# Optimization experiments

Measured on AMD Instinct MI355X. Metric: run time of the kernel, lower is better.

## Reference

```python
import jax, jax.numpy as jnp
import numpy as np

H, D = 4, 32            # heads, per-head dim (hidden = H*D = 128)
HID = H * D
OUT = 64
NC, ND, E = 50000, 50000, 400000
FC, FD = 256, 256


def setup_inputs() -> dict:
    key = jax.random.key(0)
    ks = iter(jax.random.split(key, 64))

    def n(shape, s=0.05):
        return jax.random.normal(next(ks), shape, dtype=jnp.float32) * s

    def ei(n_src, n_dst):
        return jnp.stack([jax.random.randint(next(ks), (E,), 0, n_src),
                          jax.random.randint(next(ks), (E,), 0, n_dst)]).astype(jnp.int32)

    inp = {
        'x_concept': n((NC, FC), 1.0),
        'x_doc': n((ND, FD), 1.0),
        'ei_cc': ei(NC, NC),
        'ei_dc': ei(ND, NC),
        'ei_cd': ei(NC, ND),
        # conv1 params
        'W1c': n((FC, HID)), 'b1c': n((HID,)),
        'W1d': n((FD, HID)), 'b1d': n((HID,)),
        'a1s_cc': n((H, D)), 'a1d_cc': n((H, D)),
        'a1s_dc': n((H, D)), 'a1d_dc': n((H, D)),
        'a1s_cd': n((H, D)), 'a1d_cd': n((H, D)),
        'k1W': n((HID, HID)), 'k1b': n((HID,)), 'q1': n((HID,)),
        # conv2 params
        'W2c': n((HID, HID)), 'b2c': n((HID,)),
        'W2d': n((HID, HID)), 'b2d': n((HID,)),
        'a2s_cc': n((H, D)), 'a2d_cc': n((H, D)),
        'a2s_dc': n((H, D)), 'a2d_dc': n((H, D)),
        'a2s_cd': n((H, D)), 'a2d_cd': n((H, D)),
        'k2W': n((HID, HID)), 'k2b': n((HID,)), 'q2': n((HID,)),
        # final projection
        'pW': n((HID, OUT)), 'pb': n((OUT,)),
    }
    return inp


def _seg_softmax(logit, idx, n):
    # PyG softmax: exp(x - max_per_segment) / (sum_per_segment + 1e-16)
    m = jax.ops.segment_max(logit, idx, num_segments=n)
    e = jnp.exp(logit - m[idx])
    s = jax.ops.segment_sum(e, idx, num_segments=n)
    return e / (s[idx] + 1e-16)


def _edge_att(h_src, h_dst, a_s, a_d, src, dst, n_dst):
    # h_src: [Ns,H,D]; GAT-style per-edge attention, softmax over dst
    logit = jax.nn.leaky_relu((h_src * a_s).sum(-1)[src] + (h_dst * a_d).sum(-1)[dst], 0.2)
    alpha = _seg_softmax(logit, dst, n_dst)                     # [E,H]
    out = jax.ops.segment_sum(h_src[src] * alpha[:, :, None], dst, num_segments=n_dst)
    return jax.nn.relu(out.reshape(n_dst, H * D))


def _group(outs, kW, kb, q):
    # semantic attention across relation types
    stk = jnp.stack(outs)                                       # [T,N,C]
    score = (q * jnp.tanh(stk @ kW + kb).mean(axis=1)).sum(-1)  # [T]
    w = jax.nn.softmax(score)
    return jnp.einsum('t,tnc->nc', w, stk)


def _han_layer(xc, xd, Wc, bc, Wd, bd, as_cc, ad_cc, as_dc, ad_dc, as_cd, ad_cd,
               kW, kb, q, ei_cc, ei_dc, ei_cd):
    hc = (xc @ Wc + bc).reshape(-1, H, D)
    hd = (xd @ Wd + bd).reshape(-1, H, D)
    nc, nd = hc.shape[0], hd.shape[0]
    o_cc = _edge_att(hc, hc, as_cc, ad_cc, ei_cc[0], ei_cc[1], nc)
    o_dc = _edge_att(hd, hc, as_dc, ad_dc, ei_dc[0], ei_dc[1], nc)
    o_cd = _edge_att(hc, hd, as_cd, ad_cd, ei_cd[0], ei_cd[1], nd)
    return _group([o_cc, o_dc], kW, kb, q), _group([o_cd], kW, kb, q)


def reference(x_concept, x_doc, ei_cc, ei_dc, ei_cd,
              W1c, b1c, W1d, b1d, a1s_cc, a1d_cc, a1s_dc, a1d_dc, a1s_cd, a1d_cd, k1W, k1b, q1,
              W2c, b2c, W2d, b2d, a2s_cc, a2d_cc, a2s_dc, a2d_dc, a2s_cd, a2d_cd, k2W, k2b, q2,
              pW, pb):
    c, d = _han_layer(x_concept, x_doc, W1c, b1c, W1d, b1d,
                      a1s_cc, a1d_cc, a1s_dc, a1d_dc, a1s_cd, a1d_cd,
                      k1W, k1b, q1, ei_cc, ei_dc, ei_cd)
    c, d = jax.nn.elu(c), jax.nn.elu(d)
    c, d = _han_layer(c, d, W2c, b2c, W2d, b2d,
                      a2s_cc, a2d_cc, a2s_dc, a2d_dc, a2s_cd, a2d_cd,
                      k2W, k2b, q2, ei_cc, ei_dc, ei_cd)
    c, d = jax.nn.elu(c), jax.nn.elu(d)
    pc = c @ pW + pb
    pd = d @ pW + pb
    # F.normalize(p=2) on 'concept' only
    pc = pc / jnp.maximum(jnp.linalg.norm(pc, axis=-1, keepdims=True), 1e-12)
    return pc, pd
```

## Files before the change

### kernel.cpp

```cpp
#include <hip/hip_runtime.h>
#include <hip/hip_fp16.h>
#include <cmath>

#define DEVI static __device__ __forceinline__

constexpr int HIDn = 128, OUTn = 64;
constexpr int NCn = 50000, NDn = 50000, En = 400000;
constexpr int SCAN_N = 150000, SCAN_BLK = 1024;
constexpr int SCAN_NB = (SCAN_N + SCAN_BLK - 1) / SCAN_BLK;

typedef __attribute__((ext_vector_type(8))) short bf16x8;
typedef __attribute__((ext_vector_type(4))) float f32x4;

DEVI unsigned fmap(float f) {
  int i = __float_as_int(f);
  return (i < 0) ? ~((unsigned)i) : (((unsigned)i) | 0x80000000u);
}
DEVI float fdecode(unsigned u) {
  int i = (u & 0x80000000u) ? (int)(u & 0x7fffffffu) : (int)(~u);
  return __int_as_float(i);
}

DEVI float tanh_fast(float x) {
  float e = __expf(2.f * x);
  return 1.f - __fdividef(2.f, e + 1.f);
}

DEVI unsigned short f2bf(float x) {
  unsigned u = __float_as_uint(x);
  return (unsigned short)((u + 0x7FFFu + ((u >> 16) & 1u)) >> 16);
}
DEVI float bf2f(unsigned short h) {
  unsigned u = ((unsigned)h) << 16;
  return __uint_as_float(u);
}

template<int MODE, int HALF>
DEVI void loadrow8(float* __restrict__ tmp,
                   const void* __restrict__ A, const void* __restrict__ A2,
                   float w2, float w3, size_t base)
{
  float v[8];
  if (HALF) {
    float4 raw = *(const float4*)((const __half*)A + base);
    const __half2* h2 = (const __half2*)&raw;
    #pragma unroll
    for (int j = 0; j < 4; ++j) {
      float2 f = __half22float2(h2[j]);
      v[2 * j] = f.x; v[2 * j + 1] = f.y;
    }
  } else {
    const float4* p = (const float4*)((const float*)A + base);
    float4 u0 = p[0], u1 = p[1];
    v[0] = u0.x; v[1] = u0.y; v[2] = u0.z; v[3] = u0.w;
    v[4] = u1.x; v[5] = u1.y; v[6] = u1.z; v[7] = u1.w;
  }
  if (MODE == 2) {
    float vb[8];
    if (HALF) {
      float4 raw = *(const float4*)((const __half*)A2 + base);
      const __half2* h2 = (const __half2*)&raw;
      #pragma unroll
      for (int j = 0; j < 4; ++j) {
        float2 f = __half22float2(h2[j]);
        vb[2 * j] = f.x; vb[2 * j + 1] = f.y;
      }
    } else {
      const float4* q = (const float4*)((const float*)A2 + base);
      float4 t0 = q[0], t1 = q[1];
      vb[0] = t0.x; vb[1] = t0.y; vb[2] = t0.z; vb[3] = t0.w;
      vb[4] = t1.x; vb[5] = t1.y; vb[6] = t1.z; vb[7] = t1.w;
    }
    #pragma unroll
    for (int i = 0; i < 8; ++i) v[i] = w2 * v[i] + w3 * vb[i];
  }
  if (MODE >= 1) {
    #pragma unroll
    for (int i = 0; i < 8; ++i) v[i] = (v[i] > 0.f) ? v[i] : (__expf(v[i]) - 1.f);
  }
  #pragma unroll
  for (int i = 0; i < 8; ++i) tmp[i] = v[i];
}

template<int MODE, int HALF>
DEVI bf16x8 packrow8(const void* __restrict__ A, const void* __restrict__ A2,
                     float w2, float w3, size_t base)
{
  float t[8];
  loadrow8<MODE, HALF>(t, A, A2, w2, w3, base);
  bf16x8 r;
  #pragma unroll
  for (int i = 0; i < 8; ++i) r[i] = (short)f2bf(t[i]);
  return r;
}

template<int KI, int MODEc, int MODEd, int IN16, int OUT16>
__global__ __launch_bounds__(256)
void gemm2_mfma(const void* __restrict__ Ac, const void* __restrict__ Ac2,
                const float* __restrict__ wv,
                const unsigned short* __restrict__ WcH, const unsigned short* __restrict__ WcL,
                const float* __restrict__ bc, void* __restrict__ Cc,
                const void* __restrict__ Ad,
                const unsigned short* __restrict__ WdH, const unsigned short* __restrict__ WdL,
                const float* __restrict__ bd, void* __restrict__ Cd,
                int N,
                const float* __restrict__ avc0, const float* __restrict__ avc1,
                const float* __restrict__ avc2, const float* __restrict__ avc3,
                const float* __restrict__ avd0, const float* __restrict__ avd1,
                float* __restrict__ doc0, float* __restrict__ doc1,
                float* __restrict__ doc2, float* __restrict__ doc3,
                float* __restrict__ dod0, float* __restrict__ dod1)
{
  __shared__ float As[64][36];
  __shared__ unsigned short Bh[128][40];
  __shared__ unsigned short Bl[128][40];
  constexpr int NC = KI / 32;
  const bool isC = (blockIdx.y == 0);
  const void* A  = isC ? Ac : Ad;
  const void* A2 = isC ? Ac2 : nullptr;
  const unsigned short* Wh = isC ? WcH : WdH;
  const unsigned short* Wl = isC ? WcL : WdL;
  const float* bias = isC ? bc : bd;
  void* Cv = isC ? Cc : Cd;
  float w2 = 0.f, w3 = 0.f;
  if (MODEc == 2) { if (isC) { w2 = wv[2]; w3 = wv[3]; } }

  const int tid = threadIdx.x;
  const int w = tid >> 6, lane = tid & 63;
  const int m = lane & 15, b4 = lane >> 4;
  const int row0 = blockIdx.x * 64;
  const int row0w = row0 + w * 16;

  const int rA = tid >> 2, kqA = (tid & 3) << 3;
  const int rowA = row0 + rA;
  const int cB = tid >> 1, kqB = (tid & 1) << 4;

  f32x4 acc[8];
  #pragma unroll
  for (int t = 0; t < 8; ++t) acc[t] = (f32x4){0.f, 0.f, 0.f, 0.f};

  float tA[8];
  float4 bh0, bh1, bl0, bl1;

  auto loadA = [&](int k0) {
    if (rowA < N) {
      if (isC) loadrow8<MODEc, IN16>(tA, A, A2, w2, w3, (size_t)rowA * KI + k0 + kqA);
      else     loadrow8<MODEd, IN16>(tA, A, nullptr, 0.f, 0.f, (size_t)rowA * KI + k0 + kqA);
    } else {
      #pragma unroll
      for (int i = 0; i < 8; ++i) tA[i] = 0.f;
    }
  };
  auto loadB = [&](int k0) {
    const float4* ph = (const float4*)(Wh + (size_t)cB * KI + k0 + kqB);
    const float4* pl = (const float4*)(Wl + (size_t)cB * KI + k0 + kqB);
    bh0 = ph[0]; bh1 = ph[1]; bl0 = pl[0]; bl1 = pl[1];
  };

  loadA(0);
  loadB(0);

  for (int c = 0; c < NC; ++c) {
    *(float4*)&As[rA][kqA]     = make_float4(tA[0], tA[1], tA[2], tA[3]);
    *(float4*)&As[rA][kqA + 4] = make_float4(tA[4], tA[5], tA[6], tA[7]);
    *(float4*)&Bh[cB][kqB]     = bh0;
    *(float4*)&Bh[cB][kqB + 8] = bh1;
    *(float4*)&Bl[cB][kqB]     = bl0;
    *(float4*)&Bl[cB][kqB + 8] = bl1;
    __syncthreads();

    if (c + 1 < NC) {
      loadA((c + 1) * 32);
      loadB((c + 1) * 32);
    }

    bf16x8 ah, al;
    {
      const float* ap = &As[w * 16 + m][b4 * 8];
      float4 u0 = *(const float4*)ap;
      float4 u1 = *(const float4*)(ap + 4);
      float t8[8] = {u0.x, u0.y, u0.z, u0.w, u1.x, u1.y, u1.z, u1.w};
      #pragma unroll
      for (int i = 0; i < 8; ++i) {
        unsigned short h = f2bf(t8[i]);
        ah[i] = (short)h;
        al[i] = (short)f2bf(t8[i] - bf2f(h));
      }
    }
    #pragma unroll
    for (int t = 0; t < 8; ++t) {
      const int col = t * 16 + m;
      bf16x8 bh = *(const bf16x8*)&Bh[col][b4 * 8];
      bf16x8 bl = *(const bf16x8*)&Bl[col][b4 * 8];
      acc[t] = __builtin_amdgcn_mfma_f32_16x16x32_bf16(ah, bh, acc[t], 0, 0, 0);
      acc[t] = __builtin_amdgcn_mfma_f32_16x16x32_bf16(al, bh, acc[t], 0, 0, 0);
      acc[t] = __builtin_amdgcn_mfma_f32_16x16x32_bf16(ah, bl, acc[t], 0, 0, 0);
    }
    __syncthreads();
  }

  float bt[8];
  #pragma unroll
  for (int t = 0; t < 8; ++t) bt[t] = bias[t * 16 + m];

  #pragma unroll
  for (int t = 0; t < 8; ++t) {
    const int col = t * 16 + m;
    #pragma unroll
    for (int r = 0; r < 4; ++r) {
      const int row = row0w + b4 * 4 + r;
      if (row < N) {
        float v = acc[t][r] + bt[t];
        if (OUT16) ((__half*)Cv)[(size_t)row * 128 + col] = __float2half(v);
        else       ((float*)Cv)[(size_t)row * 128 + col] = v;
      }
    }
  }

  const float* avp[4];
  float* dop[4];
  int nv;
  if (isC) {
    avp[0] = avc0; avp[1] = avc1; avp[2] = avc2; avp[3] = avc3;
    dop[0] = doc0; dop[1] = doc1; dop[2] = doc2; dop[3] = doc3; nv = 4;
  } else {
    avp[0] = avd0; avp[1] = avd1; avp[2] = avd0; avp[3] = avd1;
    dop[0] = dod0; dop[1] = dod1; dop[2] = dod0; dop[3] = dod1; nv = 2;
  }
  float avv[4][8];
  #pragma unroll
  for (int v = 0; v < 4; ++v) {
    if (v < nv) {
      #pragma unroll
      for (int t = 0; t < 8; ++t) avv[v][t] = avp[v][t * 16 + m];
    }
  }
  #pragma unroll
  for (int h = 0; h < 4; ++h) {
    #pragma unroll
    for (int v = 0; v < 4; ++v) {
      if (v < nv) {
        #pragma unroll
        for (int r = 0; r < 4; ++r) {
          float p = (acc[2 * h][r] + bt[2 * h]) * avv[v][2 * h]
                  + (acc[2 * h + 1][r] + bt[2 * h + 1]) * avv[v][2 * h + 1];
          p += __shfl_xor(p, 1);
          p += __shfl_xor(p, 2);
          p += __shfl_xor(p, 4);
          p += __shfl_xor(p, 8);
          if (m == 0) {
            const int row = row0w + b4 * 4 + r;
            if (row < N) dop[v][(size_t)row * 4 + h] = p;
          }
        }
      }
    }
  }
}

__global__ void hist3(const int* __restrict__ ei0, const int* __restrict__ ei1,
                      const int* __restrict__ ei2, int* __restrict__ deg)
{
  int gid = blockIdx.x * blockDim.x + threadIdx.x;
  if (gid >= 3 * En) return;
  int g = gid / En, e = gid - g * En;
  const int* ei = (g == 0) ? ei0 : (g == 1) ? ei1 : ei2;
  atomicAdd(&deg[g * 50000 + ei[En + e]], 1);
}

__global__ void scan_pass1(const int* __restrict__ deg, int* __restrict__ incl,
                           int* __restrict__ bsum)
{
  __shared__ int wsum[16];
  int tid = threadIdx.x;
  int gid = blockIdx.x * SCAN_BLK + tid;
  int v = (gid < SCAN_N) ? deg[gid] : 0;
  int lane = tid & 63, w = tid >> 6;
  int x = v;
  #pragma unroll
  for (int off = 1; off < 64; off <<= 1) {
    int y = __shfl_up(x, off);
    if (lane >= off) x += y;
  }
  if (lane == 63) wsum[w] = x;
  __syncthreads();
  if (tid == 0) {
    int s = 0;
    #pragma unroll
    for (int ww = 0; ww < 16; ++ww) { int t = wsum[ww]; wsum[ww] = s; s += t; }
    bsum[blockIdx.x] = s;
  }
  __syncthreads();
  x += wsum[w];
  if (gid < SCAN_N) incl[gid] = x;
}

__global__ void scan_pass2(int* __restrict__ bsum, int nb)
{
  __shared__ int wsum[16];
  int tid = threadIdx.x;
  int v = (tid < nb) ? bsum[tid] : 0;
  int lane = tid & 63, w = tid >> 6;
  int x = v;
  #pragma unroll
  for (int off = 1; off < 64; off <<= 1) {
    int y = __shfl_up(x, off);
    if (lane >= off) x += y;
  }
  if (lane == 63) wsum[w] = x;
  __syncthreads();
  if (tid == 0) {
    int s = 0;
    #pragma unroll
    for (int ww = 0; ww < 16; ++ww) { int t = wsum[ww]; wsum[ww] = s; s += t; }
  }
  __syncthreads();
  x += wsum[w];
  if (tid < nb) bsum[tid] = x - v;
}

__global__ void scan_pass3(const int* __restrict__ incl, const int* __restrict__ bsum,
                           int* __restrict__ offs)
{
  int gid = blockIdx.x * SCAN_BLK + threadIdx.x;
  if (gid == 0) offs[0] = 0;
  if (gid < SCAN_N) offs[gid + 1] = incl[gid] + bsum[gid / SCAN_BLK];
}

__global__ void fill3(const int* __restrict__ ei0, const int* __restrict__ ei1,
                      const int* __restrict__ ei2, const int* __restrict__ offs,
                      int* __restrict__ cursor, int* __restrict__ elist)
{
  int gid = blockIdx.x * blockDim.x + threadIdx.x;
  if (gid >= 3 * En) return;
  int g = gid / En, e = gid - g * En;
  const int* ei = (g == 0) ? ei0 : (g == 1) ? ei1 : ei2;
  int s = ei[e], d = g * 50000 + ei[En + e];
  int p = atomicAdd(&cursor[d], 1);
  elist[offs[d] + p] = s;
}

__global__ void wprep(const float* __restrict__ k1W, const float* __restrict__ k2W,
                      const float* __restrict__ pW,
                      const float* __restrict__ W1c, const float* __restrict__ W1d,
                      const float* __restrict__ W2c, const float* __restrict__ W2d,
                      unsigned short* kW1t, unsigned short* kW2t, unsigned short* pWt,
                      unsigned short* W1cH, unsigned short* W1cL,
                      unsigned short* W1dH, unsigned short* W1dL,
                      unsigned short* W2cH, unsigned short* W2cL,
                      unsigned short* W2dH, unsigned short* W2dL)
{
  int gid = blockIdx.x * 256 + threadIdx.x;
  if (gid < 16384) {
    int k = gid >> 7, c = gid & 127;
    kW1t[(size_t)c * 128 + k] = f2bf(k1W[gid]);
  } else if (gid < 32768) {
    int i = gid - 16384, k = i >> 7, c = i & 127;
    kW2t[(size_t)c * 128 + k] = f2bf(k2W[i]);
  } else if (gid < 40960) {
    int i = gid - 32768, k = i / 64, c = i - k * 64;
    pWt[(size_t)c * 128 + k] = f2bf(pW[i]);
  } else if (gid < 73728) {
    int i = gid - 40960, k = i >> 7, c = i & 127;
    float v = W1c[i]; unsigned short h = f2bf(v);
    W1cH[(size_t)c * 256 + k] = h;
    W1cL[(size_t)c * 256 + k] = f2bf(v - bf2f(h));
  } else if (gid < 106496) {
    int i = gid - 73728, k = i >> 7, c = i & 127;
    float v = W1d[i]; unsigned short h = f2bf(v);
    W1dH[(size_t)c * 256 + k] = h;
    W1dL[(size_t)c * 256 + k] = f2bf(v - bf2f(h));
  } else if (gid < 122880) {
    int i = gid - 106496, k = i >> 7, c = i & 127;
    float v = W2c[i]; unsigned short h = f2bf(v);
    W2cH[(size_t)c * 128 + k] = h;
    W2cL[(size_t)c * 128 + k] = f2bf(v - bf2f(h));
  } else if (gid < 139264) {
    int i = gid - 122880, k = i >> 7, c = i & 127;
    float v = W2d[i]; unsigned short h = f2bf(v);
    W2dH[(size_t)c * 128 + k] = h;
    W2dL[(size_t)c * 128 + k] = f2bf(v - bf2f(h));
  }
}

struct EdgeOp {
  const int* offs; const int* elist;
  const float* sdot; const float* ddot;
  const __half* hsrc; __half* out;
};

DEVI void csr_att_body(const EdgeOp& op, int dst, int lane)
{
  const int i0 = op.offs[dst], i1 = op.offs[dst + 1];
  const int hB = lane >> 4;
  const float ddv = op.ddot[dst * 4 + hB];
  const __half* hsrc = op.hsrc;
  const float* sdot = op.sdot;
  const int* el = op.elist;
  const int wsel = lane & 48;
  float den = 0.f, a0 = 0.f, a1 = 0.f;

  for (int base = i0; base < i1; base += 16) {
    int i = base + (lane & 15);
    int s_ = 0;
    float w = 0.f;
    if (i < i1) {
      s_ = el[i];
      float lv = sdot[s_ * 4 + hB] + ddv;
      lv = fminf(fmaxf(lv, 0.2f * lv), 80.f);
      w = __expf(lv);
    }
    float g = w;
    g += __shfl_xor(g, 1);
    g += __shfl_xor(g, 2);
    g += __shfl_xor(g, 4);
    g += __shfl_xor(g, 8);
    den += g;

    const int rem = min(16, i1 - base);
    int j = 0;
    for (; j + 2 <= rem; j += 2) {
      int sA = __shfl(s_, j);
      int sB = __shfl(s_, j + 1);
      float wA = __shfl(w, wsel | j);
      float wB = __shfl(w, wsel | (j + 1));
      float2 hA = __half22float2(*(const __half2*)(hsrc + (size_t)sA * HIDn + lane * 2));
      float2 hBv = __half22float2(*(const __half2*)(hsrc + (size_t)sB * HIDn + lane * 2));
      a0 += hA.x * wA + hBv.x * wB;
      a1 += hA.y * wA + hBv.y * wB;
    }
    if (j < rem) {
      int sA = __shfl(s_, j);
      float wA = __shfl(w, wsel | j);
      float2 hA = __half22float2(*(const __half2*)(hsrc + (size_t)sA * HIDn + lane * 2));
      a0 += hA.x * wA;
      a1 += hA.y * wA;
    }
  }
  float dinv = __fdividef(1.f, den + 1e-16f);
  __half2 o2 = __floats2half2_rn(fmaxf(a0 * dinv, 0.f), fmaxf(a1 * dinv, 0.f));
  *(__half2*)(op.out + (size_t)dst * HIDn + lane * 2) = o2;
}

__global__ __launch_bounds__(256)
void csr_att3(EdgeOp op0, EdgeOp op1, EdgeOp op2, int Ndst)
{
  int wave = (blockIdx.x * 256 + threadIdx.x) >> 6;
  if (wave >= Ndst) return;
  const int lane = threadIdx.x & 63;
  if (blockIdx.y == 0)      csr_att_body(op0, wave, lane);
  else if (blockIdx.y == 1) csr_att_body(op1, wave, lane);
  else                      csr_att_body(op2, wave, lane);
}

__global__ void edge_logit_max(const int* __restrict__ ei,
                               const float* __restrict__ sdot,
                               const float* __restrict__ ddot,
                               unsigned* __restrict__ m)
{
  int e = blockIdx.x * blockDim.x + threadIdx.x;
  if (e >= En) return;
  int s = ei[e], d = ei[En + e];
  #pragma unroll
  for (int hh = 0; hh < 4; ++hh) {
    float l = sdot[s * 4 + hh] + ddot[d * 4 + hh];
    l = (l > 0.f) ? l : 0.2f * l;
    atomicMax(&m[d * 4 + hh], fmap(l));
  }
}

__global__ void edge_exp_sum(const int* __restrict__ ei,
                             const float* __restrict__ sdot,
                             const float* __restrict__ ddot,
                             const unsigned* __restrict__ m,
                             float* __restrict__ sden,
                             float* __restrict__ ebuf)
{
  int e = blockIdx.x * blockDim.x + threadIdx.x;
  if (e >= En) return;
  int s = ei[e], d = ei[En + e];
  #pragma unroll
  for (int hh = 0; hh < 4; ++hh) {
    float l = sdot[s * 4 + hh] + ddot[d * 4 + hh];
    l = (l > 0.f) ? l : 0.2f * l;
    float ex = expf(fminf(l - fdecode(m[d * 4 + hh]), 0.f));
    ebuf[e * 4 + hh] = ex;
    atomicAdd(&sden[d * 4 + hh], ex);
  }
}

__global__ __launch_bounds__(256)
void edge_scatter(const int* __restrict__ ei, const float* __restrict__ hsrc,
                  const float* __restrict__ ebuf, const float* __restrict__ sden,
                  float* __restrict__ out)
{
  int gid  = blockIdx.x * 256 + threadIdx.x;
  int e    = gid >> 6;
  if (e >= En) return;
  int lane = gid & 63;
  int s = ei[e], d = ei[En + e];
  #pragma unroll
  for (int half = 0; half < 2; ++half) {
    int c  = lane + half * 64;
    int hh = c >> 5;
    float alpha = ebuf[e * 4 + hh] / (sden[d * 4 + hh] + 1e-16f);
    atomicAdd(&out[(size_t)d * HIDn + c], hsrc[(size_t)s * HIDn + c] * alpha);
  }
}

__global__ void relu_k(float* __restrict__ x, int n)
{
  int i = blockIdx.x * blockDim.x + threadIdx.x;
  if (i < n) x[i] = fmaxf(x[i], 0.f);
}

template<int IN16>
__global__ __launch_bounds__(256)
void score_mfma(const void* __restrict__ oA, const void* __restrict__ oB,
                const unsigned short* __restrict__ kWt,
                const float* __restrict__ kb, const float* __restrict__ q,
                int N, float* __restrict__ slots)
{
  __shared__ float partw[4];
  const void* o = blockIdx.y ? oB : oA;
  const int tid = threadIdx.x;
  const int w = tid >> 6, lane = tid & 63;
  const int row0 = (blockIdx.x * 4 + w) * 16;
  const int m = lane & 15, b = lane >> 4;
  const int arow = row0 + m;
  const bool rok = arow < N;

  const bf16x8 zfr = {0, 0, 0, 0, 0, 0, 0, 0};
  bf16x8 afr[4];
  {
    const size_t base = (size_t)arow * 128;
    #pragma unroll
    for (int ks = 0; ks < 4; ++ks) {
      if (rok) afr[ks] = packrow8<0, IN16>(o, nullptr, 0.f, 0.f, base + ks * 32 + b * 8);
      else     afr[ks] = zfr;
    }
  }

  float sum = 0.f;
  #pragma unroll
  for (int t = 0; t < 8; ++t) {
    f32x4 acc = {0.f, 0.f, 0.f, 0.f};
    const int col = t * 16 + m;
    const unsigned short* bp = kWt + (size_t)col * 128 + b * 8;
    #pragma unroll
    for (int ks = 0; ks < 4; ++ks)
      acc = __builtin_amdgcn_mfma_f32_16x16x32_bf16(afr[ks], *(const bf16x8*)(bp + ks * 32), acc, 0, 0, 0);
    const float qc = q[col], kbc = kb[col];
    #pragma unroll
    for (int r = 0; r < 4; ++r) {
      int row = row0 + b * 4 + r;
      if (row < N) sum += qc * tanh_fast(acc[r] + kbc);
    }
  }
  #pragma unroll
  for (int off = 32; off > 0; off >>= 1) sum += __shfl_down(sum, off);
  if (lane == 0) partw[w] = sum;
  __syncthreads();
  if (tid == 0)
    atomicAdd(&slots[blockIdx.y],
              (partw[0] + partw[1] + partw[2] + partw[3]) * (1.f / (float)N));
}

__global__ void softmax2_kernel(float* sb)
{
  float s0 = sb[0], s1 = sb[1];
  float mx = fmaxf(s0, s1);
  float e0 = expf(s0 - mx), e1 = expf(s1 - mx);
  float inv = 1.f / (e0 + e1);
  sb[2] = e0 * inv;
  sb[3] = e1 * inv;
}

template<int IN16>
__global__ __launch_bounds__(256)
void proj2_mfma(const void* __restrict__ fa, const void* __restrict__ fb,
                const float* __restrict__ wv, const void* __restrict__ fd,
                const unsigned short* __restrict__ pWt, const float* __restrict__ pb,
                float* __restrict__ outc, float* __restrict__ outd, int N)
{
  const bool isC = (blockIdx.y == 0);
  const int tid = threadIdx.x;
  const int w = tid >> 6, lane = tid & 63;
  const int row0 = (blockIdx.x * 4 + w) * 16;
  const int m = lane & 15, b = lane >> 4;
  const int arow = row0 + m;
  const bool rok = arow < N;
  float* out = isC ? outc : outd;

  const bf16x8 zfr = {0, 0, 0, 0, 0, 0, 0, 0};
  bf16x8 afr[4];
  {
    const size_t base = (size_t)arow * 128;
    if (isC) {
      const float w2 = wv[2], w3 = wv[3];
      #pragma unroll
      for (int ks = 0; ks < 4; ++ks) {
        if (rok) afr[ks] = packrow8<2, IN16>(fa, fb, w2, w3, base + ks * 32 + b * 8);
        else     afr[ks] = zfr;
      }
    } else {
      #pragma unroll
      for (int ks = 0; ks < 4; ++ks) {
        if (rok) afr[ks] = packrow8<1, IN16>(fd, nullptr, 0.f, 0.f, base + ks * 32 + b * 8);
        else     afr[ks] = zfr;
      }
    }
  }

  f32x4 accs[4];
  float pbc[4];
  #pragma unroll
  for (int t = 0; t < 4; ++t) {
    f32x4 acc = {0.f, 0.f, 0.f, 0.f};
    const int col = t * 16 + m;
    const unsigned short* bp = pWt + (size_t)col * 128 + b * 8;
    #pragma unroll
    for (int ks = 0; ks < 4; ++ks)
      acc = __builtin_amdgcn_mfma_f32_16x16x32_bf16(afr[ks], *(const bf16x8*)(bp + ks * 32), acc, 0, 0, 0);
    accs[t] = acc;
    pbc[t] = pb[col];
  }

  #pragma unroll
  for (int r = 0; r < 4; ++r) {
    const int row = row0 + b * 4 + r;
    float v[4];
    #pragma unroll
    for (int t = 0; t < 4; ++t) v[t] = accs[t][r] + pbc[t];
    if (isC) {
      float ss = v[0]*v[0] + v[1]*v[1] + v[2]*v[2] + v[3]*v[3];
      ss += __shfl_xor(ss, 1);
      ss += __shfl_xor(ss, 2);
      ss += __shfl_xor(ss, 4);
      ss += __shfl_xor(ss, 8);
      float inv = 1.f / fmaxf(sqrtf(ss), 1e-12f);
      #pragma unroll
      for (int t = 0; t < 4; ++t) v[t] *= inv;
    }
    if (row < N) {
      #pragma unroll
      for (int t = 0; t < 4; ++t)
        out[(size_t)row * OUTn + t * 16 + m] = v[t];
    }
  }
}

static void run_edge_fb(hipStream_t stream, const int* ei,
                        const float* sdot, const float* ddot, const float* hsrc,
                        float* outb, int Ndst,
                        unsigned* mbuf, float* sden, float* ebuf)
{
  hipMemsetAsync(mbuf, 0, (size_t)Ndst * 4 * sizeof(unsigned), stream);
  edge_logit_max<<<(En + 255) / 256, 256, 0, stream>>>(ei, sdot, ddot, mbuf);
  hipMemsetAsync(sden, 0, (size_t)Ndst * 4 * sizeof(float), stream);
  edge_exp_sum<<<(En + 255) / 256, 256, 0, stream>>>(ei, sdot, ddot, mbuf, sden, ebuf);
  hipMemsetAsync(outb, 0, (size_t)Ndst * HIDn * sizeof(float), stream);
  edge_scatter<<<((size_t)En * 64 + 255) / 256, 256, 0, stream>>>(ei, hsrc, ebuf, sden, outb);
  relu_k<<<((size_t)Ndst * HIDn + 255) / 256, 256, 0, stream>>>(outb, Ndst * HIDn);
}

extern "C" void kernel_launch(void* const* d_in, const int* in_sizes, int n_in,
                              void* d_out, int out_size, void* d_ws, size_t ws_size,
                              hipStream_t stream)
{
  const float* xc    = (const float*)d_in[0];
  const float* xd    = (const float*)d_in[1];
  const int*   ei_cc = (const int*)d_in[2];
  const int*   ei_dc = (const int*)d_in[3];
  const int*   ei_cd = (const int*)d_in[4];
  const float* W1c = (const float*)d_in[5];  const float* b1c = (const float*)d_in[6];
  const float* W1d = (const float*)d_in[7];  const float* b1d = (const float*)d_in[8];
  const float* a1s_cc = (const float*)d_in[9];  const float* a1d_cc = (const float*)d_in[10];
  const float* a1s_dc = (const float*)d_in[11]; const float* a1d_dc = (const float*)d_in[12];
  const float* a1s_cd = (const float*)d_in[13]; const float* a1d_cd = (const float*)d_in[14];
  const float* k1W = (const float*)d_in[15]; const float* k1b = (const float*)d_in[16];
  const float* q1  = (const float*)d_in[17];
  const float* W2c = (const float*)d_in[18]; const float* b2c = (const float*)d_in[19];
  const float* W2d = (const float*)d_in[20]; const float* b2d = (const float*)d_in[21];
  const float* a2s_cc = (const float*)d_in[22]; const float* a2d_cc = (const float*)d_in[23];
  const float* a2s_dc = (const float*)d_in[24]; const float* a2d_dc = (const float*)d_in[25];
  const float* a2s_cd = (const float*)d_in[26]; const float* a2d_cd = (const float*)d_in[27];
  const float* k2W = (const float*)d_in[28]; const float* k2b = (const float*)d_in[29];
  const float* q2  = (const float*)d_in[30];
  const float* pW  = (const float*)d_in[31]; const float* pb  = (const float*)d_in[32];

  float* ws = (float*)d_ws;
  const size_t NB = (size_t)NCn * HIDn;
  float* B0 = ws;
  float* B1 = ws + NB;
  float* B2 = ws + 2 * NB;
  float* B3 = ws + 3 * NB;
  float* B4 = ws + 4 * NB;
  float* sml = ws + 5 * NB;
  float* scc = sml;
  float* dcc = sml + 200000;
  float* ddc = sml + 400000;
  float* scd = sml + 600000;
  float* sdc = sml + 800000;
  float* dcd = sml + 1000000;
  float* scoreB = sml + 1200000;
  float* R0 = sml + 1200016;
  int*  R0i = (int*)R0;
  int*  offsBase  = R0i;
  int*  elistBase = R0i + 150004;
  int*  degBase   = R0i + 1350004;
  int*  cursorBase= R0i + 1500004;
  int*  inclBase  = R0i + 1650004;
  int*  bsumBase  = R0i + 1800004;
  unsigned short* kW1t = (unsigned short*)(R0i + 1801028);
  unsigned short* kW2t = (unsigned short*)(R0i + 1809220);
  unsigned short* pWt  = (unsigned short*)(R0i + 1817412);
  unsigned short* W1cH = (unsigned short*)(R0i + 1821508);
  unsigned short* W1cL = (unsigned short*)(R0i + 1837892);
  unsigned short* W1dH = (unsigned short*)(R0i + 1854276);
  unsigned short* W1dL = (unsigned short*)(R0i + 1870660);
  unsigned short* W2cH = (unsigned short*)(R0i + 1887044);
  unsigned short* W2cL = (unsigned short*)(R0i + 1895236);
  unsigned short* W2dH = (unsigned short*)(R0i + 1903428);
  unsigned short* W2dL = (unsigned short*)(R0i + 1911620);
  unsigned* mbuf = (unsigned*)R0;
  float*    sden = R0 + 200000;
  float*    ebuf = R0 + 400000;

  const size_t REQ_FLOATS = 5 * NB + 1200016 + 1919812;
  const bool useCsr = ws_size >= REQ_FLOATS * sizeof(float);

  if (useCsr) {
    hipMemsetAsync(degBase, 0, 300000 * sizeof(int), stream);
    hist3<<<(3 * En + 255) / 256, 256, 0, stream>>>(ei_cc, ei_dc, ei_cd, degBase);
    scan_pass1<<<SCAN_NB, SCAN_BLK, 0, stream>>>(degBase, inclBase, bsumBase);
    scan_pass2<<<1, SCAN_BLK, 0, stream>>>(bsumBase, SCAN_NB);
    scan_pass3<<<SCAN_NB, SCAN_BLK, 0, stream>>>(inclBase, bsumBase, offsBase);
    fill3<<<(3 * En + 255) / 256, 256, 0, stream>>>(ei_cc, ei_dc, ei_cd,
                                                    offsBase, cursorBase, elistBase);
  }
  wprep<<<(139264 + 255) / 256, 256, 0, stream>>>(k1W, k2W, pW, W1c, W1d, W2c, W2d,
                                                  kW1t, kW2t, pWt,
                                                  W1cH, W1cL, W1dH, W1dL,
                                                  W2cH, W2cL, W2dH, W2dL);

  hipMemsetAsync(scoreB, 0, 8 * sizeof(float), stream);

  const int NT64 = (NCn + 63) / 64;
  const int* offs0 = offsBase;
  const int* offs1 = offsBase + 50000;
  const int* offs2 = offsBase + 100000;

  auto edge_layer = [&](void* hc, void* hd, void* oCC, void* oDC, void* oCD) {
    if (useCsr) {
      EdgeOp o0{offs0, elistBase, scc, dcc, (const __half*)hc, (__half*)oCC};
      EdgeOp o1{offs1, elistBase, sdc, ddc, (const __half*)hd, (__half*)oDC};
      EdgeOp o2{offs2, elistBase, scd, dcd, (const __half*)hc, (__half*)oCD};
      csr_att3<<<dim3((NCn + 3) / 4, 3), 256, 0, stream>>>(o0, o1, o2, NCn);
    } else {
      run_edge_fb(stream, ei_cc, scc, dcc, (const float*)hc, (float*)oCC, NCn, mbuf, sden, ebuf);
      run_edge_fb(stream, ei_dc, sdc, ddc, (const float*)hd, (float*)oDC, NCn, mbuf, sden, ebuf);
      run_edge_fb(stream, ei_cd, scd, dcd, (const float*)hc, (float*)oCD, NDn, mbuf, sden, ebuf);
    }
  };

  if (useCsr) {
    gemm2_mfma<256, 0, 0, 0, 1><<<dim3(NT64, 2), 256, 0, stream>>>(
        xc, nullptr, nullptr, W1cH, W1cL, b1c, B0,
        xd, W1dH, W1dL, b1d, B1, NCn,
        a1s_cc, a1d_cc, a1d_dc, a1s_cd, a1s_dc, a1d_cd,
        scc, dcc, ddc, scd, sdc, dcd);
    edge_layer(B0, B1, B2, B3, B4);
    score_mfma<1><<<dim3(NT64, 2), 256, 0, stream>>>(B2, B3, kW1t, k1b, q1, NCn, scoreB);
    softmax2_kernel<<<1, 1, 0, stream>>>(scoreB);

    gemm2_mfma<128, 2, 1, 1, 1><<<dim3(NT64, 2), 256, 0, stream>>>(
        B2, B3, scoreB, W2cH, W2cL, b2c, B0,
        B4, W2dH, W2dL, b2d, B1, NCn,
        a2s_cc, a2d_cc, a2d_dc, a2s_cd, a2s_dc, a2d_cd,
        scc, dcc, ddc, scd, sdc, dcd);
    edge_layer(B0, B1, B2, B3, B4);
    score_mfma<1><<<dim3(NT64, 2), 256, 0, stream>>>(B2, B3, kW2t, k2b, q2, NCn, scoreB + 4);
    softmax2_kernel<<<1, 1, 0, stream>>>(scoreB + 4);

    proj2_mfma<1><<<dim3(NT64, 2), 256, 0, stream>>>(B2, B3, scoreB + 4, B4, pWt, pb,
                                                     (float*)d_out,
                                                     (float*)d_out + (size_t)NCn * OUTn, NCn);
  } else {
    gemm2_mfma<256, 0, 0, 0, 0><<<dim3(NT64, 2), 256, 0, stream>>>(
        xc, nullptr, nullptr, W1cH, W1cL, b1c, B0,
        xd, W1dH, W1dL, b1d, B1, NCn,
        a1s_cc, a1d_cc, a1d_dc, a1s_cd, a1s_dc, a1d_cd,
        scc, dcc, ddc, scd, sdc, dcd);
    edge_layer(B0, B1, B2, B3, B4);
    score_mfma<0><<<dim3(NT64, 2), 256, 0, stream>>>(B2, B3, kW1t, k1b, q1, NCn, scoreB);
    softmax2_kernel<<<1, 1, 0, stream>>>(scoreB);

    gemm2_mfma<128, 2, 1, 0, 0><<<dim3(NT64, 2), 256, 0, stream>>>(
        B2, B3, scoreB, W2cH, W2cL, b2c, B0,
        B4, W2dH, W2dL, b2d, B1, NCn,
        a2s_cc, a2d_cc, a2d_dc, a2s_cd, a2s_dc, a2d_cd,
        scc, dcc, ddc, scd, sdc, dcd);
    edge_layer(B0, B1, B2, B3, B4);
    score_mfma<0><<<dim3(NT64, 2), 256, 0, stream>>>(B2, B3, kW2t, k2b, q2, NCn, scoreB + 4);
    softmax2_kernel<<<1, 1, 0, stream>>>(scoreB + 4);

    proj2_mfma<0><<<dim3(NT64, 2), 256, 0, stream>>>(B2, B3, scoreB + 4, B4, pWt, pb,
                                                     (float*)d_out,
                                                     (float*)d_out + (size_t)NCn * OUTn, NCn);
  }
}
```

Measured before the change: 486.8 us.

## Pre-swizzle weights into MFMA fragment order and load B directly from global

Weight preparation now writes every bf16 weight matrix (the hi/lo split pairs, kW and pW) in per-lane MFMA fragment order. Each lane can then fetch its B operand with one coalesced 16-byte load indexed by lane. In gemm2_mfma the shared-memory staging of B (Bh/Bl tiles, their stores and prefetch registers) is removed, so B fragments are read straight from global/L2 memory inside the MFMA loop. This cuts LDS traffic and shared-memory footprint. The cost is that B reads are no longer prefetched a stage ahead and are repeated by each of the four waves, relying on cache hits.

```diff
diff --git a/kernel.cpp b/kernel.cpp
--- a/kernel.cpp
+++ b/kernel.cpp
@@ -112,14 +112,12 @@
                 float* __restrict__ dod0, float* __restrict__ dod1)
 {
   __shared__ float As[64][36];
-  __shared__ unsigned short Bh[128][40];
-  __shared__ unsigned short Bl[128][40];
   constexpr int NC = KI / 32;
   const bool isC = (blockIdx.y == 0);
   const void* A  = isC ? Ac : Ad;
   const void* A2 = isC ? Ac2 : nullptr;
-  const unsigned short* Wh = isC ? WcH : WdH;
-  const unsigned short* Wl = isC ? WcL : WdL;
+  const bf16x8* WH = (const bf16x8*)(isC ? WcH : WdH);
+  const bf16x8* WL = (const bf16x8*)(isC ? WcL : WdL);
   const float* bias = isC ? bc : bd;
   void* Cv = isC ? Cc : Cd;
   float w2 = 0.f, w3 = 0.f;
@@ -133,15 +131,12 @@
 
   const int rA = tid >> 2, kqA = (tid & 3) << 3;
   const int rowA = row0 + rA;
-  const int cB = tid >> 1, kqB = (tid & 1) << 4;
 
   f32x4 acc[8];
   #pragma unroll
   for (int t = 0; t < 8; ++t) acc[t] = (f32x4){0.f, 0.f, 0.f, 0.f};
 
   float tA[8];
-  float4 bh0, bh1, bl0, bl1;
-
   auto loadA = [&](int k0) {
     if (rowA < N) {
       if (isC) loadrow8<MODEc, IN16>(tA, A, A2, w2, w3, (size_t)rowA * KI + k0 + kqA);
@@ -151,28 +146,15 @@
       for (int i = 0; i < 8; ++i) tA[i] = 0.f;
     }
   };
-  auto loadB = [&](int k0) {
-    const float4* ph = (const float4*)(Wh + (size_t)cB * KI + k0 + kqB);
-    const float4* pl = (const float4*)(Wl + (size_t)cB * KI + k0 + kqB);
-    bh0 = ph[0]; bh1 = ph[1]; bl0 = pl[0]; bl1 = pl[1];
-  };
 
   loadA(0);
-  loadB(0);
 
   for (int c = 0; c < NC; ++c) {
     *(float4*)&As[rA][kqA]     = make_float4(tA[0], tA[1], tA[2], tA[3]);
     *(float4*)&As[rA][kqA + 4] = make_float4(tA[4], tA[5], tA[6], tA[7]);
-    *(float4*)&Bh[cB][kqB]     = bh0;
-    *(float4*)&Bh[cB][kqB + 8] = bh1;
-    *(float4*)&Bl[cB][kqB]     = bl0;
-    *(float4*)&Bl[cB][kqB + 8] = bl1;
     __syncthreads();
 
-    if (c + 1 < NC) {
-      loadA((c + 1) * 32);
-      loadB((c + 1) * 32);
-    }
+    if (c + 1 < NC) loadA((c + 1) * 32);
 
     bf16x8 ah, al;
     {
@@ -189,9 +171,9 @@
     }
     #pragma unroll
     for (int t = 0; t < 8; ++t) {
-      const int col = t * 16 + m;
-      bf16x8 bh = *(const bf16x8*)&Bh[col][b4 * 8];
-      bf16x8 bl = *(const bf16x8*)&Bl[col][b4 * 8];
+      const int fi = (c * 8 + t) * 64 + lane;
+      bf16x8 bh = WH[fi];
+      bf16x8 bl = WL[fi];
       acc[t] = __builtin_amdgcn_mfma_f32_16x16x32_bf16(ah, bh, acc[t], 0, 0, 0);
       acc[t] = __builtin_amdgcn_mfma_f32_16x16x32_bf16(al, bh, acc[t], 0, 0, 0);
       acc[t] = __builtin_amdgcn_mfma_f32_16x16x32_bf16(ah, bl, acc[t], 0, 0, 0);
@@ -352,34 +334,41 @@
 {
   int gid = blockIdx.x * 256 + threadIdx.x;
   if (gid < 16384) {
-    int k = gid >> 7, c = gid & 127;
-    kW1t[(size_t)c * 128 + k] = f2bf(k1W[gid]);
+    int i = gid, k = i >> 7, col = i & 127;
+    int ks = k >> 5, b4 = (k >> 3) & 3, j = k & 7, t = col >> 4, m = col & 15;
+    kW1t[(size_t)(((t * 4 + ks) * 64) + m + 16 * b4) * 8 + j] = f2bf(k1W[i]);
   } else if (gid < 32768) {
-    int i = gid - 16384, k = i >> 7, c = i & 127;
-    kW2t[(size_t)c * 128 + k] = f2bf(k2W[i]);
+    int i = gid - 16384, k = i >> 7, col = i & 127;
+    int ks = k >> 5, b4 = (k >> 3) & 3, j = k & 7, t = col >> 4, m = col & 15;
+    kW2t[(size_t)(((t * 4 + ks) * 64) + m + 16 * b4) * 8 + j] = f2bf(k2W[i]);
   } else if (gid < 40960) {
-    int i = gid - 32768, k = i / 64, c = i - k * 64;
-    pWt[(size_t)c * 128 + k] = f2bf(pW[i]);
+    int i = gid - 32768, k = i / 64, col = i - k * 64;
+    int ks = k >> 5, b4 = (k >> 3) & 3, j = k & 7, t = col >> 4, m = col & 15;
+    pWt[(size_t)(((t * 4 + ks) * 64) + m + 16 * b4) * 8 + j] = f2bf(pW[i]);
   } else if (gid < 73728) {
-    int i = gid - 40960, k = i >> 7, c = i & 127;
+    int i = gid - 40960, k = i >> 7, col = i & 127;
+    int c = k >> 5, b4 = (k >> 3) & 3, j = k & 7, t = col >> 4, m = col & 15;
+    size_t f = (size_t)(((c * 8 + t) * 64) + m + 16 * b4) * 8 + j;
     float v = W1c[i]; unsigned short h = f2bf(v);
-    W1cH[(size_t)c * 256 + k] = h;
-    W1cL[(size_t)c * 256 + k] = f2bf(v - bf2f(h));
+    W1cH[f] = h; W1cL[f] = f2bf(v - bf2f(h));
   } else if (gid < 106496) {
-    int i = gid - 73728, k = i >> 7, c = i & 127;
+    int i = gid - 73728, k = i >> 7, col = i & 127;
+    int c = k >> 5, b4 = (k >> 3) & 3, j = k & 7, t = col >> 4, m = col & 15;
+    size_t f = (size_t)(((c * 8 + t) * 64) + m + 16 * b4) * 8 + j;
     float v = W1d[i]; unsigned short h = f2bf(v);
-    W1dH[(size_t)c * 256 + k] = h;
-    W1dL[(size_t)c * 256 + k] = f2bf(v - bf2f(h));
+    W1dH[f] = h; W1dL[f] = f2bf(v - bf2f(h));
   } else if (gid < 122880) {
-    int i = gid - 106496, k = i >> 7, c = i & 127;
+    int i = gid - 106496, k = i >> 7, col = i & 127;
+    int c = k >> 5, b4 = (k >> 3) & 3, j = k & 7, t = col >> 4, m = col & 15;
+    size_t f = (size_t)(((c * 8 + t) * 64) + m + 16 * b4) * 8 + j;
     float v = W2c[i]; unsigned short h = f2bf(v);
-    W2cH[(size_t)c * 128 + k] = h;
-    W2cL[(size_t)c * 128 + k] = f2bf(v - bf2f(h));
+    W2cH[f] = h; W2cL[f] = f2bf(v - bf2f(h));
   } else if (gid < 139264) {
-    int i = gid - 122880, k = i >> 7, c = i & 127;
+    int i = gid - 122880, k = i >> 7, col = i & 127;
+    int c = k >> 5, b4 = (k >> 3) & 3, j = k & 7, t = col >> 4, m = col & 15;
+    size_t f = (size_t)(((c * 8 + t) * 64) + m + 16 * b4) * 8 + j;
     float v = W2d[i]; unsigned short h = f2bf(v);
-    W2dH[(size_t)c * 128 + k] = h;
-    W2dL[(size_t)c * 128 + k] = f2bf(v - bf2f(h));
+    W2dH[f] = h; W2dL[f] = f2bf(v - bf2f(h));
   }
 }
 
@@ -529,6 +518,7 @@
   const int m = lane & 15, b = lane >> 4;
   const int arow = row0 + m;
   const bool rok = arow < N;
+  const bf16x8* WT = (const bf16x8*)kWt;
 
   const bf16x8 zfr = {0, 0, 0, 0, 0, 0, 0, 0};
   bf16x8 afr[4];
@@ -546,10 +536,9 @@
   for (int t = 0; t < 8; ++t) {
     f32x4 acc = {0.f, 0.f, 0.f, 0.f};
     const int col = t * 16 + m;
-    const unsigned short* bp = kWt + (size_t)col * 128 + b * 8;
     #pragma unroll
     for (int ks = 0; ks < 4; ++ks)
-      acc = __builtin_amdgcn_mfma_f32_16x16x32_bf16(afr[ks], *(const bf16x8*)(bp + ks * 32), acc, 0, 0, 0);
+      acc = __builtin_amdgcn_mfma_f32_16x16x32_bf16(afr[ks], WT[(t * 4 + ks) * 64 + lane], acc, 0, 0, 0);
     const float qc = q[col], kbc = kb[col];
     #pragma unroll
     for (int r = 0; r < 4; ++r) {
@@ -591,6 +580,7 @@
   const int arow = row0 + m;
   const bool rok = arow < N;
   float* out = isC ? outc : outd;
+  const bf16x8* WT = (const bf16x8*)pWt;
 
   const bf16x8 zfr = {0, 0, 0, 0, 0, 0, 0, 0};
   bf16x8 afr[4];
@@ -618,10 +608,9 @@
   for (int t = 0; t < 4; ++t) {
     f32x4 acc = {0.f, 0.f, 0.f, 0.f};
     const int col = t * 16 + m;
-    const unsigned short* bp = pWt + (size_t)col * 128 + b * 8;
     #pragma unroll
     for (int ks = 0; ks < 4; ++ks)
-      acc = __builtin_amdgcn_mfma_f32_16x16x32_bf16(afr[ks], *(const bf16x8*)(bp + ks * 32), acc, 0, 0, 0);
+      acc = __builtin_amdgcn_mfma_f32_16x16x32_bf16(afr[ks], WT[(t * 4 + ks) * 64 + lane], acc, 0, 0, 0);
     accs[t] = acc;
     pbc[t] = pb[col];
   }
```

New measurement: 469.5 us. 1.04x faster.
